# Performance work log

Measured on AMD Instinct MI355X. Metric: run time of the kernel, lower is better.

The kernel has to match this reference:

```python
import jax, jax.numpy as jnp
import numpy as np

KH = KW = 3
SH = SW = 1
DH = DW = 1

def _same_padding(ih, iw):
    eff_kh = (KH - 1) * DH + 1
    eff_kw = (KW - 1) * DW + 1
    out_h = (ih + SH - 1) // SH
    out_w = (iw + SW - 1) // SW
    pad_h = max((out_h - 1) * SH + eff_kh - ih, 0)
    pad_w = max((out_w - 1) * SW + eff_kw - iw, 0)
    pad_top = pad_h // 2
    pad_bottom = pad_h - pad_top
    pad_left = pad_w // 2
    pad_right = pad_w - pad_left
    return (pad_top, pad_bottom), (pad_left, pad_right)


def setup_inputs() -> dict:
    key = jax.random.key(0)
    k1, k2, k3 = jax.random.split(key, 3)
    N, C, H, Wd = 32, 192, 56, 56
    Cout = 384
    x = jax.random.normal(k1, (N, C, H, Wd), dtype=jnp.float32)
    # linear weight (Cout, C*KH*KW) with unfold ordering (c, kh, kw) -> OIHW kernel
    W = jax.random.normal(k2, (Cout, C, KH, KW), dtype=jnp.float32) * (1.0 / np.sqrt(C * KH * KW))
    b = jax.random.normal(k3, (Cout,), dtype=jnp.float32) * 0.01
    return {"x": x, "W": W, "b": b}


def reference(x, W, b):
    # ConvLayer: F.pad('same') -> nn.Unfold -> Linear -> reshape, which is
    # mathematically a 2D conv with OIHW kernel W (unfold orders features as c,kh,kw).
    _, _, H, Wd = x.shape
    pad_hw = _same_padding(H, Wd)
    out = jax.lax.conv_general_dilated(
        x, W,
        window_strides=(SH, SW),
        padding=pad_hw,
        rhs_dilation=(DH, DW),
        dimension_numbers=("NCHW", "OIHW", "NCHW"),
    )
    return out + b[None, :, None, None]
```

## Files before the change

kernel.cpp:

```cpp
#include <hip/hip_runtime.h>
#include <cstdint>
#include <cstddef>

#define N_IMG 32
#define C_IN 192
#define HW 56
#define SPAT 3136
#define C_OUT 384
#define HP 58
#define KPOS 9
#define KTOT 1728
#define NT 27

#define BM 128
#define BN 256
#define NT_CO 3
#define NT_S  392
#define GRID_MAIN (NT_CO*NT_S)

#define BUF_EL 24576
#define B_BASE 8192

typedef __attribute__((ext_vector_type(8))) short short8;
typedef __attribute__((ext_vector_type(4))) float f32x4;

__device__ __forceinline__ unsigned short f2bf(float f) {
  union { float f; unsigned u; } v; v.f = f;
  unsigned u = v.u;
  unsigned r = (u + 0x7FFFu + ((u >> 16) & 1u)) >> 16;
  return (unsigned short)r;
}

__device__ __forceinline__ void async_load16(const void* gsrc, void* ldst) {
  __builtin_amdgcn_global_load_lds(
      (const __attribute__((address_space(1))) unsigned int*)gsrc,
      (__attribute__((address_space(3))) unsigned int*)ldst,
      16, 0, 0);
}

__device__ __forceinline__ void vm6() { asm volatile("s_waitcnt vmcnt(6)" ::: "memory"); }
__device__ __forceinline__ void vm0() { asm volatile("s_waitcnt vmcnt(0)" ::: "memory"); }

__global__ void pack_w(const float* __restrict__ W, unsigned short* __restrict__ Wp) {
  int idx = blockIdx.x*256 + threadIdx.x;
  if (idx >= C_OUT*KPOS*C_IN) return;
  int c   = idx % C_IN;
  int pos = (idx / C_IN) % KPOS;
  int co  = idx / (C_IN*KPOS);
  float v = W[((size_t)co*C_IN + c)*KPOS + pos];
  Wp[idx] = f2bf(v);
}

__global__ void zero_border(unsigned short* __restrict__ Xp) {
  int idx = blockIdx.x*256 + threadIdx.x;
  if (idx >= N_IMG*228*C_IN) return;
  int c    = idx % C_IN;
  int cell = (idx / C_IN) % 228;
  int n    = idx / (C_IN*228);
  int hh, ww;
  if (cell < 116) { hh = (cell < 58) ? 0 : 57; ww = cell % 58; }
  else { int b2 = cell - 116; ww = (b2 < 56) ? 0 : 57; hh = 1 + (b2 % 56); }
  Xp[(((size_t)n*HP + hh)*HP + ww)*C_IN + c] = 0;
}

__global__ void pack_x(const float* __restrict__ x, unsigned short* __restrict__ Xp) {
  __shared__ float tile[64*57];
  int b  = blockIdx.x;
  int cb = b % 3;
  int h  = (b/3) % HW;
  int n  = b / (3*HW);
  int tid = threadIdx.x;
  const float* src = x + (size_t)n*C_IN*SPAT + (size_t)cb*64*SPAT + h*HW;
  #pragma unroll
  for (int i = 0; i < 14; ++i) {
    int idx = i*256 + tid;
    int c = idx / HW, w = idx % HW;
    tile[c*57 + w] = src[(size_t)c*SPAT + w];
  }
  __syncthreads();
  unsigned short* dst = Xp + (((size_t)n*HP + h + 1)*HP + 1)*C_IN + cb*64;
  #pragma unroll
  for (int i = 0; i < 14; ++i) {
    int idx = i*256 + tid;
    int w = idx / 64, c = idx % 64;
    dst[(size_t)w*C_IN + c] = f2bf(tile[c*57 + w]);
  }
}

__global__ __launch_bounds__(512, 2) void conv_gemm(
    const unsigned short* __restrict__ Wp,
    const unsigned short* __restrict__ Xp,
    const float* __restrict__ bias,
    float* __restrict__ out)
{
  __shared__ __attribute__((aligned(16))) unsigned short lds[3][BUF_EL];

  int bid = blockIdx.x;
  int wg = (bid & 7) * (GRID_MAIN/8) + (bid >> 3);
  int cotile = wg % NT_CO;
  int stile  = wg / NT_CO;

  const int tid   = threadIdx.x;
  const int lane  = tid & 63;
  const int wv    = tid >> 6;
  const int wm    = wv >> 2;
  const int wn    = wv & 3;
  const int lanep = lane & 15;
  const int laneq = lane >> 4;
  const int l3    = lane >> 3;
  const int l7    = lane & 7;
  const int gsl   = (l7 ^ l3) << 3;

  const unsigned short* aSrc0;
  const unsigned short* aSrc1;
  {
    int r0 = (0*8 + wv)*8 + l3;
    aSrc0 = Wp + (size_t)(cotile*BM + r0)*KTOT + gsl;
    int r1 = (1*8 + wv)*8 + l3;
    aSrc1 = Wp + (size_t)(cotile*BM + r1)*KTOT + gsl;
  }
  const int aOff0 = (0*8 + wv)*512;
  const int aOff1 = (1*8 + wv)*512;

  const unsigned short* bSrc[4];
  int bOff[4];
  #pragma unroll
  for (int i = 0; i < 4; ++i) {
    int cbk = i*8 + wv;
    int rb  = cbk*8 + l3;
    int f   = stile*BN + rb;
    int n   = f / SPAT, sp = f % SPAT;
    bSrc[i] = Xp + (((size_t)n*HP + sp/HW)*HP + sp%HW)*C_IN + gsl;
    bOff[i] = B_BASE + cbk*512;
  }

  const int swz = (laneq ^ l7) << 3;
  const int aRd = (wm*64 + lanep)*64 + ((laneq ^ (lanep & 7)) << 3);
  const int bRd = B_BASE + (wn*64 + lanep)*64 + ((laneq ^ (lanep & 7)) << 3);
  (void)swz;

  f32x4 acc[4][4];
  #pragma unroll
  for (int mf = 0; mf < 4; ++mf)
    #pragma unroll
    for (int nf = 0; nf < 4; ++nf)
      acc[mf][nf] = (f32x4){0.f, 0.f, 0.f, 0.f};

  auto bOffOf = [](int t) {
    int pos = t / 3;
    int c0  = (t - pos*3) * 64;
    int kh  = pos / 3, kw = pos - kh*3;
    return (kh*HP + kw)*C_IN + c0;
  };

  auto stage = [&](int t, unsigned short* base) {
    const int koff = t*64;
    async_load16(aSrc0 + koff, base + aOff0);
    async_load16(aSrc1 + koff, base + aOff1);
    const int bo = bOffOf(t);
    #pragma unroll
    for (int i = 0; i < 4; ++i)
      async_load16(bSrc[i] + bo, base + bOff[i]);
  };

#define PHASE(LB, KK, STAGE_STMT, VM_STMT)                                  \
  {                                                                         \
    const unsigned short* lb_ = (LB);                                       \
    short8 av_[4], bv_[4];                                                  \
    _Pragma("unroll")                                                       \
    for (int mf = 0; mf < 4; ++mf)                                          \
      av_[mf] = *(const short8*)&lb_[(aRd + mf*1024) ^ ((KK)*32)];          \
    _Pragma("unroll")                                                       \
    for (int nf = 0; nf < 4; ++nf)                                          \
      bv_[nf] = *(const short8*)&lb_[(bRd + nf*1024) ^ ((KK)*32)];          \
    STAGE_STMT;                                                             \
    __builtin_amdgcn_sched_barrier(0);                                      \
    __builtin_amdgcn_s_barrier();                                           \
    asm volatile("s_waitcnt lgkmcnt(0)" ::: "memory");                      \
    __builtin_amdgcn_sched_barrier(0);                                      \
    __builtin_amdgcn_s_setprio(1);                                          \
    _Pragma("unroll")                                                       \
    for (int mf = 0; mf < 4; ++mf)                                          \
      _Pragma("unroll")                                                     \
      for (int nf = 0; nf < 4; ++nf)                                        \
        acc[mf][nf] = __builtin_amdgcn_mfma_f32_16x16x32_bf16(              \
            av_[mf], bv_[nf], acc[mf][nf], 0, 0, 0);                        \
    __builtin_amdgcn_s_setprio(0);                                          \
    __builtin_amdgcn_sched_barrier(0);                                      \
    VM_STMT;                                                                \
    __builtin_amdgcn_s_barrier();                                           \
  }

  unsigned short* b0 = &lds[0][0];
  unsigned short* b1 = &lds[1][0];
  unsigned short* b2 = &lds[2][0];

  stage(0, b0);
  stage(1, b1);
  vm6();
  __builtin_amdgcn_s_barrier();

  for (int t0 = 0; t0 < NT; t0 += 3) {
    PHASE(b0, 0, { if (t0 + 2 < NT) stage(t0 + 2, b2); }, );
    PHASE(b0, 1, , { if (t0     < NT-2) vm6(); else vm0(); });
    PHASE(b1, 0, { if (t0 + 3 < NT) stage(t0 + 3, b0); }, );
    PHASE(b1, 1, , { if (t0 + 1 < NT-2) vm6(); else vm0(); });
    PHASE(b2, 0, { if (t0 + 4 < NT) stage(t0 + 4, b1); }, );
    PHASE(b2, 1, , { if (t0 + 2 < NT-2) vm6(); else vm0(); });
  }
#undef PHASE

  const int coB = cotile*BM + wm*64;
  const int fB  = stile*BN + wn*64;
  #pragma unroll
  for (int nf = 0; nf < 4; ++nf) {
    int f  = fB + nf*16 + lanep;
    int n  = f / SPAT;
    int sp = f % SPAT;
    float* obase = out + (size_t)n*C_OUT*SPAT + sp;
    #pragma unroll
    for (int mf = 0; mf < 4; ++mf) {
      #pragma unroll
      for (int i = 0; i < 4; ++i) {
        int co = coB + mf*16 + laneq*4 + i;
        obase[(size_t)co*SPAT] = acc[mf][nf][i] + bias[co];
      }
    }
  }
}

__global__ void conv_naive(const float* __restrict__ x, const float* __restrict__ W,
                           const float* __restrict__ bias, float* __restrict__ out) {
  size_t idx = (size_t)blockIdx.x*256 + threadIdx.x;
  if (idx >= (size_t)N_IMG*C_OUT*SPAT) return;
  int s  = idx % SPAT;
  int co = (int)((idx / SPAT) % C_OUT);
  int n  = (int)(idx / ((size_t)SPAT*C_OUT));
  int h = s / HW, w = s % HW;
  float acc = bias[co];
  for (int c = 0; c < C_IN; ++c)
    for (int kh = 0; kh < 3; ++kh) {
      int hh = h + kh - 1;
      if (hh < 0 || hh >= HW) continue;
      for (int kw = 0; kw < 3; ++kw) {
        int ww = w + kw - 1;
        if (ww < 0 || ww >= HW) continue;
        acc += x[(((size_t)n*C_IN + c)*HW + hh)*HW + ww]
             * W[(((size_t)co*C_IN + c)*3 + kh)*3 + kw];
      }
    }
  out[idx] = acc;
}

extern "C" void kernel_launch(void* const* d_in, const int* in_sizes, int n_in,
                              void* d_out, int out_size, void* d_ws, size_t ws_size,
                              hipStream_t stream) {
  const float* x = (const float*)d_in[0];
  const float* W = (const float*)d_in[1];
  const float* b = (const float*)d_in[2];
  float* out = (float*)d_out;

  const size_t WP_ELEMS = (size_t)C_OUT*KPOS*C_IN;
  const size_t XP_ELEMS = (size_t)N_IMG*HP*HP*C_IN;
  const size_t NEED = (WP_ELEMS + XP_ELEMS)*2;

  if (ws_size >= NEED) {
    unsigned short* Wp = (unsigned short*)d_ws;
    unsigned short* Xp = Wp + WP_ELEMS;
    zero_border<<<(N_IMG*228*C_IN + 255)/256, 256, 0, stream>>>(Xp);
    pack_w<<<(int)((WP_ELEMS + 255)/256), 256, 0, stream>>>(W, Wp);
    pack_x<<<N_IMG*HW*3, 256, 0, stream>>>(x, Xp);
    conv_gemm<<<GRID_MAIN, 512, 0, stream>>>(Wp, Xp, b, out);
  } else {
    size_t total = (size_t)N_IMG*C_OUT*SPAT;
    conv_naive<<<(int)((total + 255)/256), 256, 0, stream>>>(x, W, b, out);
  }
}
```

Baseline: 190.3 us.

## Merge half-K phases per LDS buffer and halve workgroup barriers

Each LDS stage is now consumed in one phase instead of two. The phase loads both k-halves of A and B fragments up front and issues all 32 MFMAs back to back. This removes the mid-stage s_barrier, the explicit lgkmcnt wait and several sched_barriers, so the compiler can overlap LDS reads with MFMAs and fewer workgroup-wide syncs occur. The main loop is peeled so the tail stages need no runtime conditionals. In exchange, fragment register usage doubles, which may raise VGPR pressure.

```diff
diff --git a/kernel.cpp b/kernel.cpp
--- a/kernel.cpp
+++ b/kernel.cpp
@@ -111,16 +111,10 @@
   const int l7    = lane & 7;
   const int gsl   = (l7 ^ l3) << 3;
 
-  const unsigned short* aSrc0;
-  const unsigned short* aSrc1;
-  {
-    int r0 = (0*8 + wv)*8 + l3;
-    aSrc0 = Wp + (size_t)(cotile*BM + r0)*KTOT + gsl;
-    int r1 = (1*8 + wv)*8 + l3;
-    aSrc1 = Wp + (size_t)(cotile*BM + r1)*KTOT + gsl;
-  }
-  const int aOff0 = (0*8 + wv)*512;
-  const int aOff1 = (1*8 + wv)*512;
+  const unsigned short* aSrc0 = Wp + (size_t)(cotile*BM + wv*8      + l3)*KTOT + gsl;
+  const unsigned short* aSrc1 = Wp + (size_t)(cotile*BM + (wv+8)*8  + l3)*KTOT + gsl;
+  const int aOff0 = wv*512;
+  const int aOff1 = (wv+8)*512;
 
   const unsigned short* bSrc[4];
   int bOff[4];
@@ -134,10 +128,8 @@
     bOff[i] = B_BASE + cbk*512;
   }
 
-  const int swz = (laneq ^ l7) << 3;
   const int aRd = (wm*64 + lanep)*64 + ((laneq ^ (lanep & 7)) << 3);
   const int bRd = B_BASE + (wn*64 + lanep)*64 + ((laneq ^ (lanep & 7)) << 3);
-  (void)swz;
 
   f32x4 acc[4][4];
   #pragma unroll
@@ -163,32 +155,38 @@
       async_load16(bSrc[i] + bo, base + bOff[i]);
   };
 
-#define PHASE(LB, KK, STAGE_STMT, VM_STMT)                                  \
+#define PHASE(LB, STAGE_STMT, VM_STMT, DO_BAR)                              \
   {                                                                         \
     const unsigned short* lb_ = (LB);                                       \
-    short8 av_[4], bv_[4];                                                  \
-    _Pragma("unroll")                                                       \
-    for (int mf = 0; mf < 4; ++mf)                                          \
-      av_[mf] = *(const short8*)&lb_[(aRd + mf*1024) ^ ((KK)*32)];          \
-    _Pragma("unroll")                                                       \
-    for (int nf = 0; nf < 4; ++nf)                                          \
-      bv_[nf] = *(const short8*)&lb_[(bRd + nf*1024) ^ ((KK)*32)];          \
+    short8 a0_[4], b0_[4], a1_[4], b1_[4];                                  \
+    _Pragma("unroll")                                                       \
+    for (int mf = 0; mf < 4; ++mf) a0_[mf] = *(const short8*)&lb_[aRd + mf*1024];        \
+    _Pragma("unroll")                                                       \
+    for (int nf = 0; nf < 4; ++nf) b0_[nf] = *(const short8*)&lb_[bRd + nf*1024];        \
+    _Pragma("unroll")                                                       \
+    for (int mf = 0; mf < 4; ++mf) a1_[mf] = *(const short8*)&lb_[(aRd + mf*1024) ^ 32]; \
+    _Pragma("unroll")                                                       \
+    for (int nf = 0; nf < 4; ++nf) b1_[nf] = *(const short8*)&lb_[(bRd + nf*1024) ^ 32]; \
     STAGE_STMT;                                                             \
-    __builtin_amdgcn_sched_barrier(0);                                      \
-    __builtin_amdgcn_s_barrier();                                           \
-    asm volatile("s_waitcnt lgkmcnt(0)" ::: "memory");                      \
-    __builtin_amdgcn_sched_barrier(0);                                      \
     __builtin_amdgcn_s_setprio(1);                                          \
     _Pragma("unroll")                                                       \
     for (int mf = 0; mf < 4; ++mf)                                          \
       _Pragma("unroll")                                                     \
       for (int nf = 0; nf < 4; ++nf)                                        \
         acc[mf][nf] = __builtin_amdgcn_mfma_f32_16x16x32_bf16(              \
-            av_[mf], bv_[nf], acc[mf][nf], 0, 0, 0);                        \
+            a0_[mf], b0_[nf], acc[mf][nf], 0, 0, 0);                        \
+    _Pragma("unroll")                                                       \
+    for (int mf = 0; mf < 4; ++mf)                                          \
+      _Pragma("unroll")                                                     \
+      for (int nf = 0; nf < 4; ++nf)                                        \
+        acc[mf][nf] = __builtin_amdgcn_mfma_f32_16x16x32_bf16(              \
+            a1_[mf], b1_[nf], acc[mf][nf], 0, 0, 0);                        \
     __builtin_amdgcn_s_setprio(0);                                          \
-    __builtin_amdgcn_sched_barrier(0);                                      \
     VM_STMT;                                                                \
-    __builtin_amdgcn_s_barrier();                                           \
+    if (DO_BAR) {                                                           \
+      __builtin_amdgcn_s_barrier();                                         \
+      __builtin_amdgcn_sched_barrier(0);                                    \
+    }                                                                       \
   }
 
   unsigned short* b0 = &lds[0][0];
@@ -199,15 +197,16 @@
   stage(1, b1);
   vm6();
   __builtin_amdgcn_s_barrier();
-
-  for (int t0 = 0; t0 < NT; t0 += 3) {
-    PHASE(b0, 0, { if (t0 + 2 < NT) stage(t0 + 2, b2); }, );
-    PHASE(b0, 1, , { if (t0     < NT-2) vm6(); else vm0(); });
-    PHASE(b1, 0, { if (t0 + 3 < NT) stage(t0 + 3, b0); }, );
-    PHASE(b1, 1, , { if (t0 + 1 < NT-2) vm6(); else vm0(); });
-    PHASE(b2, 0, { if (t0 + 4 < NT) stage(t0 + 4, b1); }, );
-    PHASE(b2, 1, , { if (t0 + 2 < NT-2) vm6(); else vm0(); });
-  }
+  __builtin_amdgcn_sched_barrier(0);
+
+  for (int t0 = 0; t0 < 24; t0 += 3) {
+    PHASE(b0, { stage(t0 + 2, b2); }, vm6(), true);
+    PHASE(b1, { stage(t0 + 3, b0); }, vm6(), true);
+    PHASE(b2, { stage(t0 + 4, b1); }, vm6(), true);
+  }
+  PHASE(b0, { stage(26, b2); }, vm6(), true);
+  PHASE(b1, {}, vm0(), true);
+  PHASE(b2, {}, {}, false);
 #undef PHASE
 
   const int coB = cotile*BM + wm*64;
```

Measured after the change: 166.3 us. 12.6% less time.
